# Optimization experiments

Hardware: AMD Instinct MI355X
Metric: run time of the kernel (lower is better)

## Reference

```python
import jax, jax.numpy as jnp
import numpy as np

K = 9                 # num_keypoints
NA = 1                # num_anchors
NC = 1                # num_classes
NB, NH, NW = 16, 76, 76
NUM_LABELS = 2 * K + 3
MAX_T = 50
COORD_SCALE = 1.0
OBJECT_SCALE = 5.0
NOOBJECT_SCALE = 0.1
SIL_THRESH = 0.6
DIST_THRESH = 30.0
IM_W, IM_H = 640.0, 480.0
PRETRAIN_EPOCHS = 15
SHARP = 2.0           # sharpness in corner_confidences


def corner_conf(gt, pr):
    """gt, pr: [..., K, 2] normalized corner coords -> mean per-keypoint confidence [...]."""
    scale = jnp.asarray([IM_W, IM_H], dtype=gt.dtype)
    d = (gt - pr) * scale
    dist = jnp.sqrt(jnp.sum(d * d, axis=-1))                       # [..., K] pixel distance
    c = (jnp.exp(SHARP * (1.0 - dist / DIST_THRESH)) - 1.0) / (np.exp(SHARP) - 1.0)
    c = jnp.where(dist < DIST_THRESH, c, 0.0)
    return jnp.mean(c, axis=-1)


def setup_inputs() -> dict:
    key = jax.random.key(0)
    k1, k2 = jax.random.split(key)
    output = jax.random.normal(k1, (NB, NA * (2 * K + 1 + NC), NH, NW), dtype=jnp.float32)
    target = jax.random.uniform(k2, (NB, MAX_T * NUM_LABELS), dtype=jnp.float32)
    return {"output": output, "target": target, "epoch": 20}


def reference(output, target, epoch):
    out = output.reshape(NB, NA, 2 * K + 1 + NC, NH, NW)
    xs = out[:, :, 0:2 * K:2]                                      # [NB,NA,K,NH,NW]
    ys = out[:, :, 1:2 * K:2]
    xs = jnp.concatenate([jax.nn.sigmoid(xs[:, :, :1]), xs[:, :, 1:]], axis=2)  # sigmoid only kp0
    ys = jnp.concatenate([jax.nn.sigmoid(ys[:, :, :1]), ys[:, :, 1:]], axis=2)
    conf = jax.nn.sigmoid(out[:, :, 2 * K])                        # [NB,NA,NH,NW]

    # ---- predicted corners (detached, as in torch: x[i].data) ----
    xd = jax.lax.stop_gradient(xs)
    yd = jax.lax.stop_gradient(ys)
    grid_x = jnp.arange(NW, dtype=jnp.float32)
    grid_y = jnp.arange(NH, dtype=jnp.float32)
    px = (xd + grid_x[None, None, None, None, :]) / NW
    py = (yd + grid_y[None, None, None, :, None]) / NH
    pred = jnp.stack([px, py], axis=-1)                            # [NB,NA,K,NH,NW,2]
    pred = pred.transpose(0, 1, 3, 4, 2, 5).reshape(NB, NA * NH * NW, K, 2)

    # ---- ground-truth parsing ----
    tgt = jax.lax.stop_gradient(target).reshape(NB, MAX_T, NUM_LABELS)
    gt = tgt[:, :, 1:1 + 2 * K].reshape(NB, MAX_T, K, 2)           # normalized corners
    # loop breaks at first t with target[...,1]==0 -> prefix validity
    valid = jnp.cumprod((tgt[:, :, 1] != 0).astype(jnp.int32), axis=1).astype(bool)  # [NB,MAX_T]

    # ---- phase 1: silent-threshold conf mask ----
    confs = corner_conf(gt[:, :, None], pred[:, None])             # [NB,MAX_T,nAnchors]
    confs = jnp.where(valid[:, :, None], confs, 0.0)
    cur_confs = jnp.max(confs, axis=1)                             # running max, init 0 (confs>=0)
    conf_mask = jnp.where(cur_confs > SIL_THRESH, 0.0, NOOBJECT_SCALE).reshape(NB, NA, NH, NW)

    # ---- phase 2: per-GT assignment (best_n = 0) ----
    gx_all = gt[..., 0] * NW                                       # [NB,MAX_T,K]
    gy_all = gt[..., 1] * NH
    gi0 = gx_all[:, :, 0].astype(jnp.int32)                        # centroid cell
    gj0 = gy_all[:, :, 0].astype(jnp.int32)
    b_idx = jnp.broadcast_to(jnp.arange(NB)[:, None], (NB, MAX_T))
    gi = jnp.where(valid, gi0, NW)                                 # OOB index -> dropped scatter
    gj = jnp.where(valid, gj0, NH)
    a0 = jnp.zeros_like(gi)

    coord_mask = jnp.zeros((NB, NA, NH, NW)).at[b_idx, a0, gj, gi].set(1.0, mode='drop')
    conf_mask = conf_mask.at[b_idx, a0, gj, gi].set(OBJECT_SCALE, mode='drop')

    tx_vals = gx_all - gi0[..., None].astype(jnp.float32)          # [NB,MAX_T,K]
    ty_vals = gy_all - gj0[..., None].astype(jnp.float32)
    txs = jnp.zeros((NB, NA, NH, NW, K)).at[b_idx, a0, gj, gi].set(tx_vals, mode='drop')
    tys = jnp.zeros((NB, NA, NH, NW, K)).at[b_idx, a0, gj, gi].set(ty_vals, mode='drop')

    cell = jnp.clip(gj0 * NW + gi0, 0, NH * NW - 1)                # anchor-0 cell index
    pred_cells = pred.reshape(NB, NA, NH * NW, K, 2)[b_idx, 0, cell]  # [NB,MAX_T,K,2]
    tconf_vals = corner_conf(gt, pred_cells)                       # [NB,MAX_T]
    tconf = jnp.zeros((NB, NA, NH, NW)).at[b_idx, a0, gj, gi].set(tconf_vals, mode='drop')

    # ---- losses ----
    m = coord_mask[:, :, None]                                     # broadcast over K
    txs_t = jnp.moveaxis(txs, -1, 2)                               # [NB,NA,K,NH,NW]
    tys_t = jnp.moveaxis(tys, -1, 2)
    loss_x = COORD_SCALE * 0.5 * jnp.sum((xs * m - txs_t * m) ** 2)
    loss_y = COORD_SCALE * 0.5 * jnp.sum((ys * m - tys_t * m) ** 2)
    cm = jnp.sqrt(conf_mask)
    loss_conf = 0.5 * jnp.sum((conf * cm - tconf * cm) ** 2)
    if epoch > PRETRAIN_EPOCHS:
        loss = loss_x + loss_y + loss_conf
    else:
        loss = loss_x + loss_y
    return loss
```

## Files before the change

### kernel.cpp

```cpp
#include <hip/hip_runtime.h>
#include <math.h>

#define KPT 9
#define NB 16
#define NH 76
#define NW 76
#define MAX_T 50
#define NCH 20
#define NUM_LABELS 21
#define CELLS (NH*NW)
#define IM_W 640.0f
#define IM_H 480.0f
#define SX (IM_W/(float)NW)
#define SY (IM_H/(float)NH)
#define DIST_THRESH 30.0f
#define D2_THRESH (DIST_THRESH*DIST_THRESH)
#define SIL_THRESH 0.6f
#define OBJECT_SCALE 5.0f
#define NOOBJECT_SCALE 0.1f
#define PRETRAIN_EPOCHS 15
#define E2M1 6.3890560989306495f
#define CNORM (1.0f/(E2M1*9.0f))
#define CURMAX_BREAK (SIL_THRESH * E2M1 * 9.0f)
#define CNT_MIN 6

#define TSPLIT 8
#define CPB 64
#define NTHREADS (TSPLIT*64)

#define TREC 40
#define GT_FLOATS (NB*MAX_T*TREC)

__device__ __forceinline__ float sigmoidf_(float x) {
    return 1.0f / (1.0f + __expf(-x));
}

__global__ void precompute_kernel(const float* __restrict__ output,
                                  const float* __restrict__ target,
                                  float* __restrict__ wsf,
                                  int* __restrict__ W,
                                  int* __restrict__ nvA,
                                  float* __restrict__ d_out)
{
    const int b   = blockIdx.x;
    const int tid = threadIdx.x;
    const float* tgb = target + (size_t)b * MAX_T * NUM_LABELS;

    float v1 = (tid < MAX_T) ? tgb[tid * NUM_LABELS + 1] : 1.0f;
    unsigned long long zm = __ballot(v1 == 0.0f);
    int nv = (zm == 0ULL) ? MAX_T : (__ffsll((long long)zm) - 1);
    if (nv > MAX_T) nv = MAX_T;

    for (int i = tid; i < CELLS; i += 64) W[(size_t)b * CELLS + i] = -1;

    __shared__ int s_cellA[MAX_T];

    if (tid < MAX_T) {
        const float* row = tgb + tid * NUM_LABELS;
        float gx0 = row[1] * (float)NW;
        float gy0 = row[2] * (float)NH;
        int gi0 = (int)gx0;
        int gj0 = (int)gy0;
        int cellt = gj0 * NW + gi0;
        int cellc = min(max(cellt, 0), CELLS - 1);
        int hc = cellc / NW, wc = cellc % NW;
        const float* ob = output + (size_t)b * NCH * CELLS + cellc;
        float* rec = wsf + ((size_t)b * MAX_T + tid) * TREC;
        float csum = 0.0f;
        #pragma unroll
        for (int k = 0; k < KPT; ++k) {
            float gxk = row[1 + 2*k];
            float gyk = row[2 + 2*k];
            float gxp = gxk * IM_W;
            float gyp = gyk * IM_H;
            rec[2*k]      = gxp;
            rec[2*k + 1]  = gyp;
            rec[20 + 2*k] = gxk * (float)NW - (float)gi0;
            rec[21 + 2*k] = gyk * (float)NH - (float)gj0;
            float xo = ob[(2*k) * CELLS];
            float yo = ob[(2*k + 1) * CELLS];
            if (k == 0) { xo = sigmoidf_(xo); yo = sigmoidf_(yo); }
            float dx = gxp - (xo + (float)wc) * SX;
            float dy = gyp - (yo + (float)hc) * SY;
            float d2 = dx*dx + dy*dy;
            if (d2 < D2_THRESH)
                csum += __expf(2.0f - sqrtf(d2) * (2.0f / DIST_THRESH)) - 1.0f;
        }
        rec[18] = 1e18f; rec[19] = 1e18f;
        rec[38] = csum * CNORM;
        rec[39] = 0.0f;
        bool ok = (gi0 >= 0 && gi0 < NW && gj0 >= 0 && gj0 < NH) && (tid < nv);
        s_cellA[tid] = ok ? cellt : -1;
    }
    __syncthreads();
    if (tid == 0) {
        for (int t = 0; t < nv; ++t) {
            int c = s_cellA[t];
            if (c >= 0) W[(size_t)b * CELLS + c] = t;
        }
        nvA[b] = nv;
        if (b == 0) d_out[0] = 0.0f;
    }
}

__launch_bounds__(NTHREADS)
__global__ void region_loss_kernel(const float* __restrict__ output,
                                   const float* __restrict__ wsf,
                                   const int* __restrict__ W,
                                   const int* __restrict__ nvA,
                                   const int* __restrict__ epoch_p,
                                   float* __restrict__ d_out)
{
    const int tid  = threadIdx.x;
    const int wave = tid >> 6;
    const int cl   = tid & 63;
    const int b    = blockIdx.y;
    const int cell = blockIdx.x * CPB + cl;
    const bool live = (cell < CELLS);

    __shared__ float s_sil[TSPLIT][CPB];

    const int nv = nvA[b];

    float pxs[KPT], pys[KPT];
    float sil = 0.0f;
    if (live) {
        const int h = cell / NW;
        const int w = cell - h * NW;
        const float* ob = output + (size_t)b * NCH * CELLS + cell;
        #pragma unroll
        for (int k = 0; k < KPT; ++k) {
            float xo = ob[(2*k) * CELLS];
            float yo = ob[(2*k + 1) * CELLS];
            if (k == 0) { xo = sigmoidf_(xo); yo = sigmoidf_(yo); }
            pxs[k] = (xo + (float)w) * SX;
            pys[k] = (yo + (float)h) * SY;
        }

        const float* base = wsf + (size_t)b * MAX_T * TREC;
        float4 c0 = {0,0,0,0}, c1 = c0, c2 = c0, c3 = c0, c4 = c0;
        float4 n0 = c0, n1 = c0, n2 = c0, n3 = c0, n4 = c0;
        int t = wave;
        if (t < nv) {
            const float4* g = (const float4*)(base + t * TREC);
            c0 = g[0]; c1 = g[1]; c2 = g[2]; c3 = g[3]; c4 = g[4];
        }
        for (; t < nv; t += TSPLIT) {
            const int tn = t + TSPLIT;
            if (tn < nv) {
                const float4* g = (const float4*)(base + tn * TREC);
                n0 = g[0]; n1 = g[1]; n2 = g[2]; n3 = g[3]; n4 = g[4];
            }
            int cnt = 0;
            #define KP(gx, gy, k) { \
                float dx = (gx) - pxs[k]; \
                float dy = (gy) - pys[k]; \
                float d2 = __builtin_fmaf(dx, dx, dy*dy); \
                cnt += (d2 < D2_THRESH) ? 1 : 0; }
            KP(c0.x, c0.y, 0) KP(c0.z, c0.w, 1)
            KP(c1.x, c1.y, 2) KP(c1.z, c1.w, 3)
            KP(c2.x, c2.y, 4) KP(c2.z, c2.w, 5)
            KP(c3.x, c3.y, 6) KP(c3.z, c3.w, 7)
            KP(c4.x, c4.y, 8)
            #undef KP
            if (cnt >= CNT_MIN) {
                float csum = 0.0f;
                #define KQ(gx, gy, k) { \
                    float dx = (gx) - pxs[k]; \
                    float dy = (gy) - pys[k]; \
                    float d2 = __builtin_fmaf(dx, dx, dy*dy); \
                    if (d2 < D2_THRESH) \
                        csum += __expf(2.0f - sqrtf(d2) * (2.0f / DIST_THRESH)) - 1.0f; }
                KQ(c0.x, c0.y, 0) KQ(c0.z, c0.w, 1)
                KQ(c1.x, c1.y, 2) KQ(c1.z, c1.w, 3)
                KQ(c2.x, c2.y, 4) KQ(c2.z, c2.w, 5)
                KQ(c3.x, c3.y, 6) KQ(c3.z, c3.w, 7)
                KQ(c4.x, c4.y, 8)
                #undef KQ
                if (csum > CURMAX_BREAK) sil = 1.0f;
            }
            c0 = n0; c1 = n1; c2 = n2; c3 = n3; c4 = n4;
        }
    }
    s_sil[wave][cl] = sil;
    __syncthreads();

    float contrib = 0.0f;
    if (wave == 0 && live) {
        float sl = 0.0f;
        #pragma unroll
        for (int wv = 0; wv < TSPLIT; ++wv) sl = fmaxf(sl, s_sil[wv][cl]);
        const int wn = W[(size_t)b * CELLS + cell];
        const int h = cell / NW;
        const int w = cell - h * NW;
        const float* ob = output + (size_t)b * NCH * CELLS + cell;
        const float conf = sigmoidf_(ob[2*KPT * CELLS]);

        float cmask, tconf;
        if (wn >= 0) {
            const float* rec = wsf + ((size_t)b * MAX_T + wn) * TREC;
            cmask = OBJECT_SCALE;
            tconf = rec[38];
            #pragma unroll
            for (int k = 0; k < KPT; ++k) {
                float xo = pxs[k] * (1.0f/SX) - (float)w;
                float yo = pys[k] * (1.0f/SY) - (float)h;
                float dxv = xo - rec[20 + 2*k];
                float dyv = yo - rec[21 + 2*k];
                contrib += 0.5f * (dxv*dxv + dyv*dyv);
            }
        } else {
            cmask = (sl > 0.0f) ? 0.0f : NOOBJECT_SCALE;
            tconf = 0.0f;
        }
        if (epoch_p[0] > PRETRAIN_EPOCHS) {
            float d = conf - tconf;
            contrib += 0.5f * cmask * d * d;
        }
    }

    if (wave == 0) {
        #pragma unroll
        for (int off = 32; off > 0; off >>= 1)
            contrib += __shfl_down(contrib, off);
        if (cl == 0) atomicAdd(d_out, contrib);
    }
}

extern "C" void kernel_launch(void* const* d_in, const int* in_sizes, int n_in,
                              void* d_out, int out_size, void* d_ws, size_t ws_size,
                              hipStream_t stream) {
    const float* output = (const float*)d_in[0];
    const float* target = (const float*)d_in[1];
    const int*   epoch  = (const int*)d_in[2];
    float* out = (float*)d_out;

    float* wsf = (float*)d_ws;
    int*   W   = (int*)(wsf + GT_FLOATS);
    int*   nvA = W + (size_t)NB * CELLS;

    precompute_kernel<<<NB, 64, 0, stream>>>(output, target, wsf, W, nvA, out);

    dim3 grid((CELLS + CPB - 1) / CPB, NB);
    region_loss_kernel<<<grid, NTHREADS, 0, stream>>>(output, wsf, W, nvA, epoch, out);
}
```

Measured before the change: 37.22 us.

## Stage output channels and GT records in LDS; widen precompute to 512 threads

The main kernel now loads the 19 used output channels for its 64 cells cooperatively into shared memory, once per block rather than redundantly from each of the 8 waves. The ground-truth records for the batch are also staged in shared memory, which removes the per-wave register prefetch from global memory. The precompute kernel moves from 64 to 512 threads, spreading the per-keypoint confidence work across threads with shared atomics and widening the W initialisation. This adds block-wide syncs and shared-memory footprint, which may reduce occupancy.

```diff
diff --git a/kernel.cpp b/kernel.cpp
--- a/kernel.cpp
+++ b/kernel.cpp
@@ -27,6 +27,7 @@
 #define TSPLIT 8
 #define CPB 64
 #define NTHREADS (TSPLIT*64)
+#define NCH_USED 19
 
 #define TREC 40
 #define GT_FLOATS (NB*MAX_T*TREC)
@@ -35,6 +36,7 @@
     return 1.0f / (1.0f + __expf(-x));
 }
 
+__launch_bounds__(512)
 __global__ void precompute_kernel(const float* __restrict__ output,
                                   const float* __restrict__ target,
                                   float* __restrict__ wsf,
@@ -46,59 +48,69 @@
     const int tid = threadIdx.x;
     const float* tgb = target + (size_t)b * MAX_T * NUM_LABELS;
 
-    float v1 = (tid < MAX_T) ? tgb[tid * NUM_LABELS + 1] : 1.0f;
-    unsigned long long zm = __ballot(v1 == 0.0f);
-    int nv = (zm == 0ULL) ? MAX_T : (__ffsll((long long)zm) - 1);
-    if (nv > MAX_T) nv = MAX_T;
-
-    for (int i = tid; i < CELLS; i += 64) W[(size_t)b * CELLS + i] = -1;
-
-    __shared__ int s_cellA[MAX_T];
+    __shared__ int   s_nv;
+    __shared__ float s_csum[MAX_T];
+    __shared__ int   s_cellA[MAX_T];
+
+    if (tid < 64) {
+        float v1 = (tid < MAX_T) ? tgb[tid * NUM_LABELS + 1] : 1.0f;
+        unsigned long long zm = __ballot(v1 == 0.0f);
+        if (tid == 0) {
+            int fz = (zm == 0ULL) ? MAX_T : (__ffsll((long long)zm) - 1);
+            s_nv = fz < MAX_T ? fz : MAX_T;
+        }
+    }
+    if (tid < MAX_T) s_csum[tid] = 0.0f;
+    for (int i = tid; i < CELLS; i += 512) W[(size_t)b * CELLS + i] = -1;
+    __syncthreads();
+
+    if (tid < MAX_T * KPT) {
+        const int t = tid / KPT;
+        const int k = tid - t * KPT;
+        const float* row = tgb + t * NUM_LABELS;
+        float gxk = row[1 + 2*k];
+        float gyk = row[2 + 2*k];
+        int gi0 = (int)(row[1] * (float)NW);
+        int gj0 = (int)(row[2] * (float)NH);
+        float* rec = wsf + ((size_t)b * MAX_T + t) * TREC;
+        float gxp = gxk * IM_W;
+        float gyp = gyk * IM_H;
+        rec[2*k]      = gxp;
+        rec[2*k + 1]  = gyp;
+        rec[20 + 2*k] = gxk * (float)NW - (float)gi0;
+        rec[21 + 2*k] = gyk * (float)NH - (float)gj0;
+        int cellc = min(max(gj0 * NW + gi0, 0), CELLS - 1);
+        int hc = cellc / NW, wc = cellc - hc * NW;
+        const float* ob = output + (size_t)b * NCH * CELLS + cellc;
+        float xo = ob[(2*k) * CELLS];
+        float yo = ob[(2*k + 1) * CELLS];
+        if (k == 0) { xo = sigmoidf_(xo); yo = sigmoidf_(yo); }
+        float dx = gxp - (xo + (float)wc) * SX;
+        float dy = gyp - (yo + (float)hc) * SY;
+        float d2 = dx*dx + dy*dy;
+        if (d2 < D2_THRESH)
+            atomicAdd(&s_csum[t], __expf(2.0f - sqrtf(d2) * (2.0f / DIST_THRESH)) - 1.0f);
+    }
+    __syncthreads();
 
     if (tid < MAX_T) {
         const float* row = tgb + tid * NUM_LABELS;
-        float gx0 = row[1] * (float)NW;
-        float gy0 = row[2] * (float)NH;
-        int gi0 = (int)gx0;
-        int gj0 = (int)gy0;
-        int cellt = gj0 * NW + gi0;
-        int cellc = min(max(cellt, 0), CELLS - 1);
-        int hc = cellc / NW, wc = cellc % NW;
-        const float* ob = output + (size_t)b * NCH * CELLS + cellc;
+        int gi0 = (int)(row[1] * (float)NW);
+        int gj0 = (int)(row[2] * (float)NH);
         float* rec = wsf + ((size_t)b * MAX_T + tid) * TREC;
-        float csum = 0.0f;
-        #pragma unroll
-        for (int k = 0; k < KPT; ++k) {
-            float gxk = row[1 + 2*k];
-            float gyk = row[2 + 2*k];
-            float gxp = gxk * IM_W;
-            float gyp = gyk * IM_H;
-            rec[2*k]      = gxp;
-            rec[2*k + 1]  = gyp;
-            rec[20 + 2*k] = gxk * (float)NW - (float)gi0;
-            rec[21 + 2*k] = gyk * (float)NH - (float)gj0;
-            float xo = ob[(2*k) * CELLS];
-            float yo = ob[(2*k + 1) * CELLS];
-            if (k == 0) { xo = sigmoidf_(xo); yo = sigmoidf_(yo); }
-            float dx = gxp - (xo + (float)wc) * SX;
-            float dy = gyp - (yo + (float)hc) * SY;
-            float d2 = dx*dx + dy*dy;
-            if (d2 < D2_THRESH)
-                csum += __expf(2.0f - sqrtf(d2) * (2.0f / DIST_THRESH)) - 1.0f;
-        }
         rec[18] = 1e18f; rec[19] = 1e18f;
-        rec[38] = csum * CNORM;
+        rec[38] = s_csum[tid] * CNORM;
         rec[39] = 0.0f;
-        bool ok = (gi0 >= 0 && gi0 < NW && gj0 >= 0 && gj0 < NH) && (tid < nv);
-        s_cellA[tid] = ok ? cellt : -1;
+        bool ok = (gi0 >= 0 && gi0 < NW && gj0 >= 0 && gj0 < NH) && (tid < s_nv);
+        s_cellA[tid] = ok ? (gj0 * NW + gi0) : -1;
     }
     __syncthreads();
     if (tid == 0) {
-        for (int t = 0; t < nv; ++t) {
+        for (int t = 0; t < s_nv; ++t) {
             int c = s_cellA[t];
             if (c >= 0) W[(size_t)b * CELLS + c] = t;
         }
-        nvA[b] = nv;
+        nvA[b] = s_nv;
         if (b == 0) d_out[0] = 0.0f;
     }
 }
@@ -115,53 +127,61 @@
     const int wave = tid >> 6;
     const int cl   = tid & 63;
     const int b    = blockIdx.y;
-    const int cell = blockIdx.x * CPB + cl;
+    const int cellb = blockIdx.x * CPB;
+    const int cell = cellb + cl;
     const bool live = (cell < CELLS);
 
-    __shared__ float s_sil[TSPLIT][CPB];
+    __shared__ float  s_ch[NCH_USED][CPB];
+    __shared__ float4 s_gt4[MAX_T][5];
+    __shared__ float  s_sil[TSPLIT][CPB];
+
+    {
+        const float* obase = output + (size_t)b * NCH * CELLS + cellb;
+        for (int idx = tid; idx < NCH_USED * CPB; idx += NTHREADS) {
+            int ch = idx >> 6, c = idx & 63;
+            s_ch[ch][c] = (cellb + c < CELLS) ? obase[(size_t)ch * CELLS + c] : 0.0f;
+        }
+        const float4* gbase = (const float4*)(wsf + (size_t)b * MAX_T * TREC);
+        for (int idx = tid; idx < MAX_T * 5; idx += NTHREADS) {
+            int t = idx / 5, q = idx - t * 5;
+            s_gt4[t][q] = gbase[t * (TREC/4) + q];
+        }
+    }
+    __syncthreads();
 
     const int nv = nvA[b];
+    const int h = cell / NW;
+    const int w = cell - h * NW;
 
     float pxs[KPT], pys[KPT];
+    #pragma unroll
+    for (int k = 0; k < KPT; ++k) {
+        float xo = s_ch[2*k][cl];
+        float yo = s_ch[2*k + 1][cl];
+        if (k == 0) { xo = sigmoidf_(xo); yo = sigmoidf_(yo); }
+        pxs[k] = (xo + (float)w) * SX;
+        pys[k] = (yo + (float)h) * SY;
+    }
+
     float sil = 0.0f;
     if (live) {
-        const int h = cell / NW;
-        const int w = cell - h * NW;
-        const float* ob = output + (size_t)b * NCH * CELLS + cell;
-        #pragma unroll
-        for (int k = 0; k < KPT; ++k) {
-            float xo = ob[(2*k) * CELLS];
-            float yo = ob[(2*k + 1) * CELLS];
-            if (k == 0) { xo = sigmoidf_(xo); yo = sigmoidf_(yo); }
-            pxs[k] = (xo + (float)w) * SX;
-            pys[k] = (yo + (float)h) * SY;
-        }
-
-        const float* base = wsf + (size_t)b * MAX_T * TREC;
-        float4 c0 = {0,0,0,0}, c1 = c0, c2 = c0, c3 = c0, c4 = c0;
-        float4 n0 = c0, n1 = c0, n2 = c0, n3 = c0, n4 = c0;
-        int t = wave;
-        if (t < nv) {
-            const float4* g = (const float4*)(base + t * TREC);
-            c0 = g[0]; c1 = g[1]; c2 = g[2]; c3 = g[3]; c4 = g[4];
-        }
-        for (; t < nv; t += TSPLIT) {
-            const int tn = t + TSPLIT;
-            if (tn < nv) {
-                const float4* g = (const float4*)(base + tn * TREC);
-                n0 = g[0]; n1 = g[1]; n2 = g[2]; n3 = g[3]; n4 = g[4];
-            }
+        for (int t = wave; t < nv; t += TSPLIT) {
+            float4 q0 = s_gt4[t][0];
+            float4 q1 = s_gt4[t][1];
+            float4 q2 = s_gt4[t][2];
+            float4 q3 = s_gt4[t][3];
+            float4 q4 = s_gt4[t][4];
             int cnt = 0;
             #define KP(gx, gy, k) { \
                 float dx = (gx) - pxs[k]; \
                 float dy = (gy) - pys[k]; \
                 float d2 = __builtin_fmaf(dx, dx, dy*dy); \
                 cnt += (d2 < D2_THRESH) ? 1 : 0; }
-            KP(c0.x, c0.y, 0) KP(c0.z, c0.w, 1)
-            KP(c1.x, c1.y, 2) KP(c1.z, c1.w, 3)
-            KP(c2.x, c2.y, 4) KP(c2.z, c2.w, 5)
-            KP(c3.x, c3.y, 6) KP(c3.z, c3.w, 7)
-            KP(c4.x, c4.y, 8)
+            KP(q0.x, q0.y, 0) KP(q0.z, q0.w, 1)
+            KP(q1.x, q1.y, 2) KP(q1.z, q1.w, 3)
+            KP(q2.x, q2.y, 4) KP(q2.z, q2.w, 5)
+            KP(q3.x, q3.y, 6) KP(q3.z, q3.w, 7)
+            KP(q4.x, q4.y, 8)
             #undef KP
             if (cnt >= CNT_MIN) {
                 float csum = 0.0f;
@@ -171,15 +191,14 @@
                     float d2 = __builtin_fmaf(dx, dx, dy*dy); \
                     if (d2 < D2_THRESH) \
                         csum += __expf(2.0f - sqrtf(d2) * (2.0f / DIST_THRESH)) - 1.0f; }
-                KQ(c0.x, c0.y, 0) KQ(c0.z, c0.w, 1)
-                KQ(c1.x, c1.y, 2) KQ(c1.z, c1.w, 3)
-                KQ(c2.x, c2.y, 4) KQ(c2.z, c2.w, 5)
-                KQ(c3.x, c3.y, 6) KQ(c3.z, c3.w, 7)
-                KQ(c4.x, c4.y, 8)
+                KQ(q0.x, q0.y, 0) KQ(q0.z, q0.w, 1)
+                KQ(q1.x, q1.y, 2) KQ(q1.z, q1.w, 3)
+                KQ(q2.x, q2.y, 4) KQ(q2.z, q2.w, 5)
+                KQ(q3.x, q3.y, 6) KQ(q3.z, q3.w, 7)
+                KQ(q4.x, q4.y, 8)
                 #undef KQ
                 if (csum > CURMAX_BREAK) sil = 1.0f;
             }
-            c0 = n0; c1 = n1; c2 = n2; c3 = n3; c4 = n4;
         }
     }
     s_sil[wave][cl] = sil;
@@ -191,10 +210,7 @@
         #pragma unroll
         for (int wv = 0; wv < TSPLIT; ++wv) sl = fmaxf(sl, s_sil[wv][cl]);
         const int wn = W[(size_t)b * CELLS + cell];
-        const int h = cell / NW;
-        const int w = cell - h * NW;
-        const float* ob = output + (size_t)b * NCH * CELLS + cell;
-        const float conf = sigmoidf_(ob[2*KPT * CELLS]);
+        const float conf = sigmoidf_(s_ch[18][cl]);
 
         float cmask, tconf;
         if (wn >= 0) {
@@ -239,7 +255,7 @@
     int*   W   = (int*)(wsf + GT_FLOATS);
     int*   nvA = W + (size_t)NB * CELLS;
 
-    precompute_kernel<<<NB, 64, 0, stream>>>(output, target, wsf, W, nvA, out);
+    precompute_kernel<<<NB, 512, 0, stream>>>(output, target, wsf, W, nvA, out);
 
     dim3 grid((CELLS + CPB - 1) / CPB, NB);
     region_loss_kernel<<<grid, NTHREADS, 0, stream>>>(output, wsf, W, nvA, epoch, out);
```

Result: faster. 34.75 us (-6.6%).
